# Optimization experiments

Hardware: AMD Instinct MI355X
Metric: run time of the kernel (lower is better)

Reference implementation:

```python
import jax, jax.numpy as jnp
import numpy as np

TEMPERATURE = 0.2
EPS = 1e-12

def _l2norm(v, axis=-1):
    return v / jnp.maximum(jnp.linalg.norm(v, axis=axis, keepdims=True), EPS)

def setup_inputs() -> dict:
    key = jax.random.key(0)
    k1, k2, k3, k4, k5 = jax.random.split(key, 5)
    B, D, P, K = 4096, 256, 100, 10
    return {
        "x": jax.random.normal(k1, (B, D), dtype=jnp.float32),
        "x_aug": jax.random.normal(k2, (B, D), dtype=jnp.float32),
        "proto_w": jax.random.normal(k3, (P, D), dtype=jnp.float32),
        "hard_q": jax.random.randint(k4, (2, B), 0, P, dtype=jnp.int32),
        "neg_q": jax.random.randint(k5, (2, B, K), 0, P, dtype=jnp.int32),
    }

def reference(x, x_aug, proto_w, hard_q, neg_q):
    # graphcl.loss_cal with args.hard_selection=True, args.proto_dist=True,
    # args.sample_dist=False. The original O(n^2) python loops are vectorized
    # as gathers/broadcasts; math is identical.
    B = x.shape[0]
    P = proto_w.shape[0]
    out1 = _l2norm(x)                      # [B, D]
    out2 = _l2norm(x_aug)                  # [B, D]
    out = jnp.concatenate([out1, out2], 0) # [2B, D]
    n = 2 * B

    sim = jnp.exp(out @ out.T / TEMPERATURE)          # [2B, 2B]
    eye = jnp.eye(n, dtype=bool)

    hq = hard_q.reshape(-1)                # [2B]  (concat of the two views)
    nq = neg_q.reshape(n, -1)              # [2B, K]

    # hard_selection: mask[i,j] = (i != j) and (hard_q[j] in neg_q[i]).
    # Build per-prototype membership [2B, P], then gather columns by hq[j].
    mem_proto = (nq[:, :, None] == jnp.arange(P, dtype=nq.dtype)[None, None, :]).any(1)  # [2B, P]
    member = jnp.take(mem_proto, hq, axis=1)          # [2B, 2B]
    mask = (~eye) & member

    # proto_dist reweighting (prototypes used via .data, i.e. detached).
    w = _l2norm(jax.lax.stop_gradient(proto_w))       # [P, D]
    pd = 1.0 - w @ w.T                                # [P, P]
    rw = jnp.where(eye, 0.0, pd[hq[:, None], hq[None, :]])  # [2B, 2B]
    rmin = rw.min(axis=1, keepdims=True)
    rmax = rw.max(axis=1, keepdims=True)
    rw = (rw - rmin) / (rmax - rmin)
    # NOTE: torch broadcasts (2B,2B) - (2B,) along columns -> mu[None, :]
    mu = rw.mean(axis=1)
    std = jnp.std(rw, axis=1, ddof=1)  # torch.std default: unbiased
    rw = jnp.exp((rw - mu[None, :]) ** 2 / (2.0 * std[None, :] ** 2))
    sim = sim * rw

    pos = jnp.exp(jnp.sum(out1 * out2, axis=-1) / TEMPERATURE)  # [B]
    pos = jnp.concatenate([pos, pos], 0)                        # [2B]
    # masked_select(...).sum(dim=-1) in the original sums ALL kept entries.
    denom = jnp.sum(jnp.where(mask, sim, 0.0))
    loss = jnp.mean(-jnp.log(pos / denom))
    return loss
```

## Files before the change

kernel.cpp:

```cpp
#include <hip/hip_runtime.h>
#include <cmath>

#define BB   4096
#define DD   256
#define NN   8192
#define PP   100
#define KK   10

typedef float f32x16 __attribute__((ext_vector_type(16)));
typedef long  lx2    __attribute__((ext_vector_type(2)));

constexpr size_t OFF_DPART = 0;
constexpr size_t OFF_PPART = 512;
constexpr size_t OFF_CNT   = 1536;
constexpr size_t OFF_MU    = 2048;
constexpr size_t OFF_SD    = 2560;
constexpr size_t OFF_RWN   = 3072;
constexpr size_t OFF_PI    = 43072;
constexpr size_t OFF_INVP  = 75840;
constexpr size_t OFF_HQP   = 108608;
constexpr size_t OFF_CTABT = 141376;
constexpr size_t OFF_G     = 3418176;


__global__ __launch_bounds__(1024) void prep_kernel(
    const int* __restrict__ hq, int* __restrict__ cnt,
    int* __restrict__ pi, int* __restrict__ invp, int* __restrict__ hqp,
    double* __restrict__ dpart, double* __restrict__ ppart) {
    __shared__ int h[16][PP];
    __shared__ int cur[PP];
    const int t = threadIdx.x;
    const int wv = t >> 6;
    h[t & 15][t >> 4] = 0;
    if (t < 576) h[(t + 1024) & 15][(t + 1024) >> 4] = 0;
    if (t < 64) { dpart[t] = 0.0; ppart[t] = 0.0; }
    __syncthreads();
#pragma unroll
    for (int r = 0; r < 8; ++r) atomicAdd(&h[wv][hq[r * 1024 + t]], 1);
    __syncthreads();
    if (t < PP) {
        int s = 0;
#pragma unroll
        for (int w = 0; w < 16; ++w) s += h[w][t];
        cnt[t] = s;
        h[0][t] = s;
    }
    __syncthreads();
    if (t == 0) {
        int run = 0;
        for (int c = 0; c < PP; ++c) { cur[c] = run; run += h[0][c]; }
    }
    __syncthreads();
#pragma unroll
    for (int r = 0; r < 8; ++r) {
        const int i = r * 1024 + t;
        const int c = hq[i];
        const int d = atomicAdd(&cur[c], 1);
        pi[d] = i;
        hqp[d] = c;
        invp[i] = d;
    }
}

__global__ __launch_bounds__(256) void norm_protopd_kernel(
    const float* __restrict__ x, const float* __restrict__ xa,
    const float* __restrict__ pw, const int* __restrict__ invp,
    const int* __restrict__ cnt, char* __restrict__ Gpb, double* __restrict__ ppart,
    float* __restrict__ rwn, float* __restrict__ mu, float* __restrict__ sd) {
    const int blk = blockIdx.x;
    const int t = threadIdx.x;
    if (blk < 1024) {
        const int wv = t >> 6, lane = t & 63;
        const int i = blk * 4 + wv;
        const float4 v1 = *(const float4*)(x  + (size_t)i * DD + lane * 4);
        const float4 v2 = *(const float4*)(xa + (size_t)i * DD + lane * 4);
        float a = v1.x * v1.x + v1.y * v1.y + v1.z * v1.z + v1.w * v1.w;
        float b = v2.x * v2.x + v2.y * v2.y + v2.z * v2.z + v2.w * v2.w;
        float c = v1.x * v2.x + v1.y * v2.y + v1.z * v2.z + v1.w * v2.w;
#pragma unroll
        for (int off = 32; off > 0; off >>= 1) {
            a += __shfl_xor(a, off);
            b += __shfl_xor(b, off);
            c += __shfl_xor(c, off);
        }
        const float d1 = fmaxf(sqrtf(a), 1e-12f), i1 = 1.0f / d1;
        const float d2 = fmaxf(sqrtf(b), 1e-12f), i2 = 1.0f / d2;
        const int p1 = invp[i];
        const int p2 = invp[i + BB];
        int w1 = __builtin_amdgcn_cvt_pk_fp8_f32(v1.x * i1, v1.y * i1, 0, false);
        w1 = __builtin_amdgcn_cvt_pk_fp8_f32(v1.z * i1, v1.w * i1, w1, true);
        int w2 = __builtin_amdgcn_cvt_pk_fp8_f32(v2.x * i2, v2.y * i2, 0, false);
        w2 = __builtin_amdgcn_cvt_pk_fp8_f32(v2.z * i2, v2.w * i2, w2, true);
        const int q = lane >> 3, halfsel = (lane >> 1) & 1, pairsel = (lane >> 2) & 1;
        const int bo = pairsel * 8 + 4 * (lane & 1);
        const size_t a1 = (size_t)((p1 >> 5) * 8192 + q * 1024 +
                                   (halfsel * 32 + (p1 & 31)) * 16 + bo);
        const size_t a2 = (size_t)((p2 >> 5) * 8192 + q * 1024 +
                                   (halfsel * 32 + (p2 & 31)) * 16 + bo);
        *(int*)(Gpb + a1) = w1;
        *(int*)(Gpb + a2) = w2;
        if (lane == 0) atomicAdd(&ppart[i & 63], (double)(c * i1 * i2));
    } else {
        const int a = blk - 1024;
        __shared__ alignas(16) float wa[DD];
        __shared__ float pdrow[PP];
        __shared__ float r4[4];
        float av = pw[(size_t)a * DD + t];
        float ss = av * av;
#pragma unroll
        for (int off = 32; off > 0; off >>= 1) ss += __shfl_down(ss, off);
        if ((t & 63) == 0) r4[t >> 6] = ss;
        __syncthreads();
        const float na = fmaxf(sqrtf(r4[0] + r4[1] + r4[2] + r4[3]), 1e-12f);
        wa[t] = av / na;
        __syncthreads();
        if (t < PP) {
            const float4* wc = (const float4*)(pw + (size_t)t * DD);
            float dot = 0.f, nb = 0.f;
#pragma unroll 4
            for (int k = 0; k < 64; ++k) {
                const float4 w = wc[k];
                const float4 u = *(const float4*)(wa + 4 * k);
                dot += u.x * w.x + u.y * w.y + u.z * w.z + u.w * w.w;
                nb += w.x * w.x + w.y * w.y + w.z * w.z + w.w * w.w;
            }
            pdrow[t] = 1.0f - dot / fmaxf(sqrtf(nb), 1e-12f);
        }
        __syncthreads();
        if (t < 64) {
            const int lane = t;
            float vmin = 0.f, vmax = 0.f;
            for (int b = lane; b < PP; b += 64) {
                int cc = cnt[b] - (b == a ? 1 : 0);
                if (cc > 0) {
                    float v = pdrow[b];
                    vmin = fminf(vmin, v);
                    vmax = fmaxf(vmax, v);
                }
            }
#pragma unroll
            for (int off = 32; off > 0; off >>= 1) {
                vmin = fminf(vmin, __shfl_xor(vmin, off));
                vmax = fmaxf(vmax, __shfl_xor(vmax, off));
            }
            const float den = vmax - vmin;
            const float inv = (den > 0.f) ? 1.f / den : 0.f;
            double s1 = 0.0, s2 = 0.0;
            for (int b = lane; b < PP; b += 64) {
                float v = (pdrow[b] - vmin) * inv;
                rwn[a * PP + b] = v;
                int cc = cnt[b] - (b == a ? 1 : 0);
                if (cc > 0) { double dv = v; s1 += cc * dv; s2 += cc * dv * dv; }
            }
            if (lane == 0) { double v0 = (0.0 - (double)vmin) * inv; s1 += v0; s2 += v0 * v0; }
#pragma unroll
            for (int off = 32; off > 0; off >>= 1) {
                s1 += __shfl_xor(s1, off);
                s2 += __shfl_xor(s2, off);
            }
            if (lane == 0) {
                double m = s1 / (double)NN;
                double var = (s2 - (double)NN * m * m) / (double)(NN - 1);
                mu[a] = (float)m;
                sd[a] = (float)sqrt(fmax(var, 0.0));
            }
        }
    }
}

__global__ __launch_bounds__(256) void ctab_kernel(
    const int* __restrict__ pi, const int* __restrict__ hqp, const int* __restrict__ nq,
    const float* __restrict__ rwn, const float* __restrict__ mu, const float* __restrict__ sd,
    float* __restrict__ CtabT) {
    const int p0 = blockIdx.x * 32;
    const int t = threadIdx.x;
    __shared__ unsigned long long bits[32][2];
    __shared__ int cls[32];
    __shared__ float smu[PP], ssd[PP];
    if (t < 32) {
        const int p = p0 + t;
        const int* row = nq + (size_t)pi[p] * KK;
        unsigned long long b0 = 0, b1 = 0;
#pragma unroll
        for (int k = 0; k < KK; ++k) {
            int c = row[k];
            if (c < 64) b0 |= 1ull << c; else b1 |= 1ull << (c - 64);
        }
        bits[t][0] = b0;
        bits[t][1] = b1;
        cls[t] = hqp[p];
    }
    if (t < PP) { smu[t] = mu[t]; ssd[t] = sd[t]; }
    __syncthreads();
    for (int idx = t; idx < 32 * PP; idx += 256) {
        const int c = idx >> 5;
        const int pl = idx & 31;
        const bool m = (c < 64) ? ((bits[pl][0] >> c) & 1) : ((bits[pl][1] >> (c - 64)) & 1);
        float v = 0.f;
        if (m) {
            float d = rwn[cls[pl] * PP + c] - smu[c];
            float s = ssd[c];
            v = expf(d * d / (2.0f * s * s));
        }
        CtabT[(size_t)c * NN + p0 + pl] = v;
    }
}

__device__ __forceinline__ void gload_lds16(void* g, void* l) {
    typedef __attribute__((address_space(1))) void* as1_void_p;
    typedef __attribute__((address_space(3))) void* as3_void_p;
    __builtin_amdgcn_global_load_lds((as1_void_p)g, (as3_void_p)l, 16, 0, 0);
}

__global__ __launch_bounds__(256) void sim_kernel(
    const char* __restrict__ Gpb, const int* __restrict__ hqp,
    const float* __restrict__ CtabT, double* __restrict__ dpart) {
    const int xcd = blockIdx.x & 7;
    int idx = blockIdx.x >> 3;
    if (idx >= 496 + (xcd >> 1) * 16) return;
    int bj = 0, bi = 0;
#pragma unroll
    for (int q = 0; q < 16; ++q) {
        const int bjq = xcd + 8 * q;
        const int c = (bjq >> 1) + 1;
        if (idx < c) { bj = bjq; bi = idx; break; }
        idx -= c;
    }

    const int t = threadIdx.x;
    const int lane = t & 63;
    const int wv = t >> 6;
    const int i0w = bi * 128 + wv * 32;
    const int j0 = bj * 64;

    __shared__ alignas(16) char lB[16384];

    const char* pa = Gpb + (size_t)(i0w >> 5) * 8192 + lane * 16;
    lx2 a[8];
#pragma unroll
    for (int q = 0; q < 8; ++q) a[q] = *(const lx2*)(pa + q * 1024);

    char* gB = const_cast<char*>(Gpb) + (size_t)(j0 >> 5) * 8192;
#pragma unroll
    for (int s = 0; s < 4; ++s) {
        const int off = (s * 4 + wv) * 1024;
        gload_lds16(gB + off + lane * 16, lB + off);
    }

    const int cl = lane & 31, h = lane >> 5;
    const int col0 = j0 + cl;
    const int col1 = j0 + 32 + cl;
    const int cls0 = hqp[col0];
    const int cls1 = hqp[col1];

    __syncthreads();

    f32x16 acc[2] = {};
#pragma unroll
    for (int q = 0; q < 8; ++q) {
        const lx2 b0 = *(const lx2*)(lB + q * 1024 + lane * 16);
        const lx2 b1 = *(const lx2*)(lB + 8192 + q * 1024 + lane * 16);
        acc[0] = __builtin_amdgcn_mfma_f32_32x32x16_fp8_fp8(a[q].x, b0.x, acc[0], 0, 0, 0);
        acc[1] = __builtin_amdgcn_mfma_f32_32x32x16_fp8_fp8(a[q].x, b1.x, acc[1], 0, 0, 0);
        acc[0] = __builtin_amdgcn_mfma_f32_32x32x16_fp8_fp8(a[q].y, b0.y, acc[0], 0, 0, 0);
        acc[1] = __builtin_amdgcn_mfma_f32_32x32x16_fp8_fp8(a[q].y, b1.y, acc[1], 0, 0, 0);
    }

    const float* ct0 = CtabT + (size_t)cls0 * NN;
    const float* ct1 = CtabT + (size_t)cls1 * NN;
    float partial = 0.f;
#pragma unroll
    for (int g = 0; g < 4; ++g) {
        const int rbase = i0w + 8 * g + 4 * h;
        const int4 rc = *(const int4*)(hqp + rbase);
        const float4 cf0 = *(const float4*)(ct0 + rbase);
        const float4 cf1 = *(const float4*)(ct1 + rbase);
        const float* f0 = (const float*)&cf0;
        const float* f1 = (const float*)&cf1;
        const int rcv[4] = {rc.x, rc.y, rc.z, rc.w};
#pragma unroll
        for (int r = 0; r < 4; ++r) {
            const int row = rbase + r;
            const float* ctr = CtabT + (size_t)rcv[r] * NN;
            const float c20 = ctr[col0];
            const float c21 = ctr[col1];
            const float e0 = __expf(acc[0][4 * g + r] * 5.0f);
            const float e1 = __expf(acc[1][4 * g + r] * 5.0f);
            partial += (row < col0) ? e0 * (f0[r] + c20) : 0.f;
            partial += (row < col1) ? e1 * (f1[r] + c21) : 0.f;
        }
    }
#pragma unroll
    for (int off = 32; off > 0; off >>= 1) partial += __shfl_down(partial, off);
    __shared__ float wsum[4];
    if (lane == 0) wsum[wv] = partial;
    __syncthreads();
    if (t == 0)
        atomicAdd(&dpart[blockIdx.x & 63], (double)(wsum[0] + wsum[1] + wsum[2] + wsum[3]));
}

__global__ void finalize_kernel(const double* __restrict__ dpart,
                                const double* __restrict__ ppart, float* __restrict__ out) {
    const int lane = threadIdx.x;
    double d = dpart[lane], p = ppart[lane];
#pragma unroll
    for (int off = 32; off > 0; off >>= 1) {
        d += __shfl_down(d, off);
        p += __shfl_down(p, off);
    }
    if (lane == 0) out[0] = (float)(log(d) - p * (5.0 / 4096.0));
}

extern "C" void kernel_launch(void* const* d_in, const int* in_sizes, int n_in,
                              void* d_out, int out_size, void* d_ws, size_t ws_size,
                              hipStream_t stream) {
    const float* x  = (const float*)d_in[0];
    const float* xa = (const float*)d_in[1];
    const float* pw = (const float*)d_in[2];
    const int* hq   = (const int*)d_in[3];
    const int* nq   = (const int*)d_in[4];
    float* out      = (float*)d_out;

    char* ws = (char*)d_ws;
    double* dpart = (double*)(ws + OFF_DPART);
    double* ppart = (double*)(ws + OFF_PPART);
    int* cnt      = (int*)(ws + OFF_CNT);
    float* mu     = (float*)(ws + OFF_MU);
    float* sd     = (float*)(ws + OFF_SD);
    float* rwn    = (float*)(ws + OFF_RWN);
    int* pi       = (int*)(ws + OFF_PI);
    int* invp     = (int*)(ws + OFF_INVP);
    int* hqp      = (int*)(ws + OFF_HQP);
    float* CtabT  = (float*)(ws + OFF_CTABT);
    char* Gpb     = (char*)(ws + OFF_G);

    prep_kernel<<<1, 1024, 0, stream>>>(hq, cnt, pi, invp, hqp, dpart, ppart);
    norm_protopd_kernel<<<1124, 256, 0, stream>>>(x, xa, pw, invp, cnt, Gpb, ppart,
                                                  rwn, mu, sd);
    ctab_kernel<<<NN / 32, 256, 0, stream>>>(pi, hqp, nq, rwn, mu, sd, CtabT);
    sim_kernel<<<8 * 544, 256, 0, stream>>>(Gpb, hqp, CtabT, dpart);
    finalize_kernel<<<1, 64, 0, stream>>>(dpart, ppart, out);
}
```

Before: 143.6 us.

## Widen sim tiles to 128x128, fuse finalize via ticket, move scatter into norm

The sim kernel now computes 128x128 upper-triangular tiles instead of 128x64, so each B tile loaded into LDS is reused across four accumulators and fewer blocks are launched. The separate finalize launch is replaced by a last-block ticket reduction inside the sim kernel. The permutation scatter moves from the single-block prep kernel into the normalization kernel using global atomics. In exchange, each block uses more LDS and registers, and the permutation order within a class becomes nondeterministic.

```diff
diff --git a/kernel.cpp b/kernel.cpp
--- a/kernel.cpp
+++ b/kernel.cpp
@@ -12,28 +12,29 @@
 
 constexpr size_t OFF_DPART = 0;
 constexpr size_t OFF_PPART = 512;
+constexpr size_t OFF_TICKET= 1024;
 constexpr size_t OFF_CNT   = 1536;
 constexpr size_t OFF_MU    = 2048;
 constexpr size_t OFF_SD    = 2560;
 constexpr size_t OFF_RWN   = 3072;
 constexpr size_t OFF_PI    = 43072;
-constexpr size_t OFF_INVP  = 75840;
+constexpr size_t OFF_CUR   = 75840;
 constexpr size_t OFF_HQP   = 108608;
 constexpr size_t OFF_CTABT = 141376;
 constexpr size_t OFF_G     = 3418176;
 
 
 __global__ __launch_bounds__(1024) void prep_kernel(
-    const int* __restrict__ hq, int* __restrict__ cnt,
-    int* __restrict__ pi, int* __restrict__ invp, int* __restrict__ hqp,
-    double* __restrict__ dpart, double* __restrict__ ppart) {
+    const int* __restrict__ hq, int* __restrict__ cnt, int* __restrict__ cur,
+    double* __restrict__ dpart, double* __restrict__ ppart, int* __restrict__ ticket) {
     __shared__ int h[16][PP];
-    __shared__ int cur[PP];
+    __shared__ int sc[PP];
     const int t = threadIdx.x;
     const int wv = t >> 6;
     h[t & 15][t >> 4] = 0;
     if (t < 576) h[(t + 1024) & 15][(t + 1024) >> 4] = 0;
     if (t < 64) { dpart[t] = 0.0; ppart[t] = 0.0; }
+    if (t == 1023) ticket[0] = 0;
     __syncthreads();
 #pragma unroll
     for (int r = 0; r < 8; ++r) atomicAdd(&h[wv][hq[r * 1024 + t]], 1);
@@ -43,28 +44,21 @@
 #pragma unroll
         for (int w = 0; w < 16; ++w) s += h[w][t];
         cnt[t] = s;
-        h[0][t] = s;
+        sc[t] = s;
     }
     __syncthreads();
     if (t == 0) {
         int run = 0;
-        for (int c = 0; c < PP; ++c) { cur[c] = run; run += h[0][c]; }
-    }
-    __syncthreads();
-#pragma unroll
-    for (int r = 0; r < 8; ++r) {
-        const int i = r * 1024 + t;
-        const int c = hq[i];
-        const int d = atomicAdd(&cur[c], 1);
-        pi[d] = i;
-        hqp[d] = c;
-        invp[i] = d;
-    }
+        for (int c = 0; c < PP; ++c) { int v = sc[c]; sc[c] = run; run += v; }
+    }
+    __syncthreads();
+    if (t < PP) cur[t] = sc[t];
 }
 
 __global__ __launch_bounds__(256) void norm_protopd_kernel(
     const float* __restrict__ x, const float* __restrict__ xa,
-    const float* __restrict__ pw, const int* __restrict__ invp,
+    const float* __restrict__ pw, const int* __restrict__ hq,
+    int* __restrict__ cur, int* __restrict__ pi, int* __restrict__ hqp,
     const int* __restrict__ cnt, char* __restrict__ Gpb, double* __restrict__ ppart,
     float* __restrict__ rwn, float* __restrict__ mu, float* __restrict__ sd) {
     const int blk = blockIdx.x;
@@ -72,6 +66,15 @@
     if (blk < 1024) {
         const int wv = t >> 6, lane = t & 63;
         const int i = blk * 4 + wv;
+        int p1 = 0, p2 = 0;
+        if (lane == 0) {
+            const int c1 = hq[i];
+            const int c2 = hq[i + BB];
+            p1 = atomicAdd(&cur[c1], 1);
+            p2 = atomicAdd(&cur[c2], 1);
+            pi[p1] = i;        hqp[p1] = c1;
+            pi[p2] = i + BB;   hqp[p2] = c2;
+        }
         const float4 v1 = *(const float4*)(x  + (size_t)i * DD + lane * 4);
         const float4 v2 = *(const float4*)(xa + (size_t)i * DD + lane * 4);
         float a = v1.x * v1.x + v1.y * v1.y + v1.z * v1.z + v1.w * v1.w;
@@ -85,8 +88,8 @@
         }
         const float d1 = fmaxf(sqrtf(a), 1e-12f), i1 = 1.0f / d1;
         const float d2 = fmaxf(sqrtf(b), 1e-12f), i2 = 1.0f / d2;
-        const int p1 = invp[i];
-        const int p2 = invp[i + BB];
+        p1 = __shfl(p1, 0);
+        p2 = __shfl(p2, 0);
         int w1 = __builtin_amdgcn_cvt_pk_fp8_f32(v1.x * i1, v1.y * i1, 0, false);
         w1 = __builtin_amdgcn_cvt_pk_fp8_f32(v1.z * i1, v1.w * i1, w1, true);
         int w2 = __builtin_amdgcn_cvt_pk_fp8_f32(v2.x * i2, v2.y * i2, 0, false);
@@ -212,103 +215,123 @@
     __builtin_amdgcn_global_load_lds((as1_void_p)g, (as3_void_p)l, 16, 0, 0);
 }
 
+#define SIM_BLOCKS 2304
+
 __global__ __launch_bounds__(256) void sim_kernel(
     const char* __restrict__ Gpb, const int* __restrict__ hqp,
-    const float* __restrict__ CtabT, double* __restrict__ dpart) {
-    const int xcd = blockIdx.x & 7;
-    int idx = blockIdx.x >> 3;
-    if (idx >= 496 + (xcd >> 1) * 16) return;
-    int bj = 0, bi = 0;
-#pragma unroll
-    for (int q = 0; q < 16; ++q) {
-        const int bjq = xcd + 8 * q;
-        const int c = (bjq >> 1) + 1;
-        if (idx < c) { bj = bjq; bi = idx; break; }
-        idx -= c;
-    }
-
+    const float* __restrict__ CtabT, double* __restrict__ dpart,
+    double* __restrict__ ppart, int* __restrict__ ticket, float* __restrict__ out) {
+    __shared__ alignas(16) char lB[32768];
+    __shared__ float wsum[4];
+    __shared__ int lastflag;
     const int t = threadIdx.x;
     const int lane = t & 63;
     const int wv = t >> 6;
-    const int i0w = bi * 128 + wv * 32;
-    const int j0 = bj * 64;
-
-    __shared__ alignas(16) char lB[16384];
-
-    const char* pa = Gpb + (size_t)(i0w >> 5) * 8192 + lane * 16;
-    lx2 a[8];
-#pragma unroll
-    for (int q = 0; q < 8; ++q) a[q] = *(const lx2*)(pa + q * 1024);
-
-    char* gB = const_cast<char*>(Gpb) + (size_t)(j0 >> 5) * 8192;
-#pragma unroll
-    for (int s = 0; s < 4; ++s) {
-        const int off = (s * 4 + wv) * 1024;
-        gload_lds16(gB + off + lane * 16, lB + off);
-    }
-
-    const int cl = lane & 31, h = lane >> 5;
-    const int col0 = j0 + cl;
-    const int col1 = j0 + 32 + cl;
-    const int cls0 = hqp[col0];
-    const int cls1 = hqp[col1];
-
-    __syncthreads();
-
-    f32x16 acc[2] = {};
-#pragma unroll
-    for (int q = 0; q < 8; ++q) {
-        const lx2 b0 = *(const lx2*)(lB + q * 1024 + lane * 16);
-        const lx2 b1 = *(const lx2*)(lB + 8192 + q * 1024 + lane * 16);
-        acc[0] = __builtin_amdgcn_mfma_f32_32x32x16_fp8_fp8(a[q].x, b0.x, acc[0], 0, 0, 0);
-        acc[1] = __builtin_amdgcn_mfma_f32_32x32x16_fp8_fp8(a[q].x, b1.x, acc[1], 0, 0, 0);
-        acc[0] = __builtin_amdgcn_mfma_f32_32x32x16_fp8_fp8(a[q].y, b0.y, acc[0], 0, 0, 0);
-        acc[1] = __builtin_amdgcn_mfma_f32_32x32x16_fp8_fp8(a[q].y, b1.y, acc[1], 0, 0, 0);
-    }
-
-    const float* ct0 = CtabT + (size_t)cls0 * NN;
-    const float* ct1 = CtabT + (size_t)cls1 * NN;
-    float partial = 0.f;
-#pragma unroll
-    for (int g = 0; g < 4; ++g) {
-        const int rbase = i0w + 8 * g + 4 * h;
-        const int4 rc = *(const int4*)(hqp + rbase);
-        const float4 cf0 = *(const float4*)(ct0 + rbase);
-        const float4 cf1 = *(const float4*)(ct1 + rbase);
-        const float* f0 = (const float*)&cf0;
-        const float* f1 = (const float*)&cf1;
-        const int rcv[4] = {rc.x, rc.y, rc.z, rc.w};
-#pragma unroll
-        for (int r = 0; r < 4; ++r) {
-            const int row = rbase + r;
-            const float* ctr = CtabT + (size_t)rcv[r] * NN;
-            const float c20 = ctr[col0];
-            const float c21 = ctr[col1];
-            const float e0 = __expf(acc[0][4 * g + r] * 5.0f);
-            const float e1 = __expf(acc[1][4 * g + r] * 5.0f);
-            partial += (row < col0) ? e0 * (f0[r] + c20) : 0.f;
-            partial += (row < col1) ? e1 * (f1[r] + c21) : 0.f;
-        }
-    }
-#pragma unroll
-    for (int off = 32; off > 0; off >>= 1) partial += __shfl_down(partial, off);
-    __shared__ float wsum[4];
-    if (lane == 0) wsum[wv] = partial;
-    __syncthreads();
-    if (t == 0)
-        atomicAdd(&dpart[blockIdx.x & 63], (double)(wsum[0] + wsum[1] + wsum[2] + wsum[3]));
-}
-
-__global__ void finalize_kernel(const double* __restrict__ dpart,
-                                const double* __restrict__ ppart, float* __restrict__ out) {
-    const int lane = threadIdx.x;
-    double d = dpart[lane], p = ppart[lane];
-#pragma unroll
-    for (int off = 32; off > 0; off >>= 1) {
-        d += __shfl_down(d, off);
-        p += __shfl_down(p, off);
-    }
-    if (lane == 0) out[0] = (float)(log(d) - p * (5.0 / 4096.0));
+    const int xcd = blockIdx.x & 7;
+    int idx = blockIdx.x >> 3;
+    const bool active = (idx < 8 * xcd + 232);
+
+    if (active) {
+        int bj = 0, bi = 0;
+#pragma unroll
+        for (int q = 0; q < 8; ++q) {
+            const int bjq = xcd + 8 * q;
+            const int c = bjq + 1;
+            if (idx < c) { bj = bjq; bi = idx; break; }
+            idx -= c;
+        }
+
+        const int i0w = bi * 128 + wv * 32;
+        const int j0 = bj * 128;
+
+        const char* pa = Gpb + (size_t)(i0w >> 5) * 8192 + lane * 16;
+        lx2 a[8];
+#pragma unroll
+        for (int q = 0; q < 8; ++q) a[q] = *(const lx2*)(pa + q * 1024);
+
+        char* gB = const_cast<char*>(Gpb) + (size_t)bj * 32768;
+#pragma unroll
+        for (int s = 0; s < 8; ++s) {
+            const int off = (s * 4 + wv) * 1024;
+            gload_lds16(gB + off + lane * 16, lB + off);
+        }
+
+        const int cl = lane & 31, h = lane >> 5;
+        int cols[4];
+        const float* ct[4];
+#pragma unroll
+        for (int cg = 0; cg < 4; ++cg) {
+            cols[cg] = j0 + cg * 32 + cl;
+            ct[cg] = CtabT + (size_t)hqp[cols[cg]] * NN;
+        }
+
+        __syncthreads();
+
+        f32x16 acc[4] = {};
+#pragma unroll
+        for (int q = 0; q < 8; ++q) {
+            const lx2 b0 = *(const lx2*)(lB +         q * 1024 + lane * 16);
+            const lx2 b1 = *(const lx2*)(lB +  8192 + q * 1024 + lane * 16);
+            const lx2 b2 = *(const lx2*)(lB + 16384 + q * 1024 + lane * 16);
+            const lx2 b3 = *(const lx2*)(lB + 24576 + q * 1024 + lane * 16);
+            acc[0] = __builtin_amdgcn_mfma_f32_32x32x16_fp8_fp8(a[q].x, b0.x, acc[0], 0, 0, 0);
+            acc[1] = __builtin_amdgcn_mfma_f32_32x32x16_fp8_fp8(a[q].x, b1.x, acc[1], 0, 0, 0);
+            acc[2] = __builtin_amdgcn_mfma_f32_32x32x16_fp8_fp8(a[q].x, b2.x, acc[2], 0, 0, 0);
+            acc[3] = __builtin_amdgcn_mfma_f32_32x32x16_fp8_fp8(a[q].x, b3.x, acc[3], 0, 0, 0);
+            acc[0] = __builtin_amdgcn_mfma_f32_32x32x16_fp8_fp8(a[q].y, b0.y, acc[0], 0, 0, 0);
+            acc[1] = __builtin_amdgcn_mfma_f32_32x32x16_fp8_fp8(a[q].y, b1.y, acc[1], 0, 0, 0);
+            acc[2] = __builtin_amdgcn_mfma_f32_32x32x16_fp8_fp8(a[q].y, b2.y, acc[2], 0, 0, 0);
+            acc[3] = __builtin_amdgcn_mfma_f32_32x32x16_fp8_fp8(a[q].y, b3.y, acc[3], 0, 0, 0);
+        }
+
+        float partial = 0.f;
+#pragma unroll
+        for (int g = 0; g < 4; ++g) {
+            const int rbase = i0w + 8 * g + 4 * h;
+            const int4 rc = *(const int4*)(hqp + rbase);
+            float4 cf[4];
+#pragma unroll
+            for (int cg = 0; cg < 4; ++cg)
+                cf[cg] = *(const float4*)(ct[cg] + rbase);
+            const int rcv[4] = {rc.x, rc.y, rc.z, rc.w};
+#pragma unroll
+            for (int r = 0; r < 4; ++r) {
+                const int row = rbase + r;
+                const float* ctr = CtabT + (size_t)rcv[r] * NN;
+#pragma unroll
+                for (int cg = 0; cg < 4; ++cg) {
+                    const float c2 = ctr[cols[cg]];
+                    const float* f = (const float*)&cf[cg];
+                    const float e = __expf(acc[cg][4 * g + r] * 5.0f);
+                    partial += (row < cols[cg]) ? e * (f[r] + c2) : 0.f;
+                }
+            }
+        }
+#pragma unroll
+        for (int off = 32; off > 0; off >>= 1) partial += __shfl_down(partial, off);
+        if (lane == 0) wsum[wv] = partial;
+        __syncthreads();
+        if (t == 0)
+            atomicAdd(&dpart[blockIdx.x & 63],
+                      (double)(wsum[0] + wsum[1] + wsum[2] + wsum[3]));
+    }
+
+    if (t == 0) {
+        __threadfence();
+        const int old = atomicAdd(ticket, 1);
+        lastflag = (old == SIM_BLOCKS - 1) ? 1 : 0;
+    }
+    __syncthreads();
+    if (lastflag && t < 64) {
+        double d = atomicAdd(&dpart[t], 0.0);
+        double p = atomicAdd(&ppart[t], 0.0);
+#pragma unroll
+        for (int off = 32; off > 0; off >>= 1) {
+            d += __shfl_down(d, off);
+            p += __shfl_down(p, off);
+        }
+        if (t == 0) out[0] = (float)(log(d) - p * (5.0 / 4096.0));
+    }
 }
 
 extern "C" void kernel_launch(void* const* d_in, const int* in_sizes, int n_in,
@@ -324,20 +347,20 @@
     char* ws = (char*)d_ws;
     double* dpart = (double*)(ws + OFF_DPART);
     double* ppart = (double*)(ws + OFF_PPART);
+    int* ticket   = (int*)(ws + OFF_TICKET);
     int* cnt      = (int*)(ws + OFF_CNT);
     float* mu     = (float*)(ws + OFF_MU);
     float* sd     = (float*)(ws + OFF_SD);
     float* rwn    = (float*)(ws + OFF_RWN);
     int* pi       = (int*)(ws + OFF_PI);
-    int* invp     = (int*)(ws + OFF_INVP);
+    int* cur      = (int*)(ws + OFF_CUR);
     int* hqp      = (int*)(ws + OFF_HQP);
     float* CtabT  = (float*)(ws + OFF_CTABT);
     char* Gpb     = (char*)(ws + OFF_G);
 
-    prep_kernel<<<1, 1024, 0, stream>>>(hq, cnt, pi, invp, hqp, dpart, ppart);
-    norm_protopd_kernel<<<1124, 256, 0, stream>>>(x, xa, pw, invp, cnt, Gpb, ppart,
-                                                  rwn, mu, sd);
+    prep_kernel<<<1, 1024, 0, stream>>>(hq, cnt, cur, dpart, ppart, ticket);
+    norm_protopd_kernel<<<1124, 256, 0, stream>>>(x, xa, pw, hq, cur, pi, hqp, cnt,
+                                                  Gpb, ppart, rwn, mu, sd);
     ctab_kernel<<<NN / 32, 256, 0, stream>>>(pi, hqp, nq, rwn, mu, sd, CtabT);
-    sim_kernel<<<8 * 544, 256, 0, stream>>>(Gpb, hqp, CtabT, dpart);
-    finalize_kernel<<<1, 64, 0, stream>>>(dpart, ppart, out);
-}
+    sim_kernel<<<SIM_BLOCKS, 256, 0, stream>>>(Gpb, hqp, CtabT, dpart, ppart, ticket, out);
+}
```

Result: slower. 201.7 us (+40.5%).
